# Optimization experiments

Measured on AMD Instinct MI355X. Metric: run time of the kernel, lower is better.

The kernel has to match this reference:

```python
import jax, jax.numpy as jnp
import numpy as np

DIM = 2048
MAX_LEN = 8192
EPS = 1e-6


def rms_norm(x, w):
    # x / sqrt(mean(x^2) + eps) * w
    rms = jnp.sqrt(jnp.mean(x * x, axis=-1, keepdims=True) + EPS)
    return x / rms * w


def setup_inputs() -> dict:
    key = jax.random.key(0)
    ks = jax.random.split(key, 12)
    s = 0.02  # weight init scale
    return {
        "x": jax.random.normal(ks[0], (1, DIM), jnp.float32),
        "cacheK": jax.random.normal(ks[1], (MAX_LEN, DIM), jnp.float32),
        "cacheV": jax.random.normal(ks[2], (MAX_LEN, DIM), jnp.float32),
        "attn_norm_w": jnp.ones((DIM,), jnp.float32),
        "q_w": jax.random.normal(ks[3], (DIM, DIM), jnp.float32) * s,
        "q_b": jnp.zeros((DIM,), jnp.float32),
        "k_w": jax.random.normal(ks[4], (DIM, DIM), jnp.float32) * s,
        "k_b": jnp.zeros((DIM,), jnp.float32),
        "v_w": jax.random.normal(ks[5], (DIM, DIM), jnp.float32) * s,
        "v_b": jnp.zeros((DIM,), jnp.float32),
        "o_w": jax.random.normal(ks[6], (DIM, DIM), jnp.float32) * s,
        "o_b": jnp.zeros((DIM,), jnp.float32),
        "mlp_norm_w": jnp.ones((DIM,), jnp.float32),
        "fc1_w": jax.random.normal(ks[7], (4 * DIM, DIM), jnp.float32) * s,
        "fc1_b": jnp.zeros((4 * DIM,), jnp.float32),
        "fc2_w": jax.random.normal(ks[8], (DIM, 4 * DIM), jnp.float32) * s,
        "fc2_b": jnp.zeros((DIM,), jnp.float32),
        "pos": 4096,
    }


def reference(x, cacheK, cacheV, attn_norm_w, q_w, q_b, k_w, k_b, v_w, v_b,
              o_w, o_b, mlp_norm_w, fc1_w, fc1_b, fc2_w, fc2_b, pos):
    dim = x.shape[-1]
    xn = rms_norm(x, attn_norm_w)                     # [1, d]
    q = xn @ q_w.T + q_b                              # [1, d]
    k = xn @ k_w.T + k_b
    v = xn @ v_w.T + v_b
    cacheK = cacheK.at[pos].set(k[0])                 # scatter write new KV
    cacheV = cacheV.at[pos].set(v[0])
    # attention over cache[:pos+1] (pos is a static Python int)
    scores = (cacheK[:pos + 1] @ q[0]) / np.sqrt(dim)  # [pos+1]
    probs = jax.nn.softmax(scores, axis=0)
    attn = (probs @ cacheV[:pos + 1])[None, :]        # [1, d]
    x = x + attn @ o_w.T + o_b
    hn = rms_norm(x, mlp_norm_w)
    h = jax.nn.gelu(hn @ fc1_w.T + fc1_b, approximate=False)  # exact erf GELU
    x = x + h @ fc2_w.T + fc2_b
    return x
```

## Files before the change

kernel.cpp:

```cpp
#include <hip/hip_runtime.h>

#define DIMN 2048
#define HDIM 8192

#define WS_XN   0
#define WS_Q    2048
#define WS_ATTN 4096
#define WS_X1   6144
#define WS_HN   8192
#define WS_H    10240
#define WS_SC   18432
#define WS_PR   26624

__device__ __forceinline__ float dot4(float4 w, float4 a) {
    return w.x * a.x + w.y * a.y + w.z * a.z + w.w * a.w;
}

__device__ __forceinline__ float waveSum(float v) {
#pragma unroll
    for (int off = 32; off > 0; off >>= 1) v += __shfl_down(v, off, 64);
    return v;
}

__global__ void k_rms1(const float* __restrict__ x, const float* __restrict__ w,
                       float* __restrict__ ws) {
    __shared__ float red[5];
    int tid = threadIdx.x;
    float4 a = reinterpret_cast<const float4*>(x)[tid * 2];
    float4 b = reinterpret_cast<const float4*>(x)[tid * 2 + 1];
    float ss = a.x * a.x + a.y * a.y + a.z * a.z + a.w * a.w +
               b.x * b.x + b.y * b.y + b.z * b.z + b.w * b.w;
    ss = waveSum(ss);
    int wave = tid >> 6, lane = tid & 63;
    if (lane == 0) red[wave] = ss;
    __syncthreads();
    if (tid == 0) red[4] = rsqrtf((red[0] + red[1] + red[2] + red[3]) / (float)DIMN + 1e-6f);
    __syncthreads();
    float scale = red[4];
    float4 wa = reinterpret_cast<const float4*>(w)[tid * 2];
    float4 wb = reinterpret_cast<const float4*>(w)[tid * 2 + 1];
    float4 o0 = make_float4(a.x * scale * wa.x, a.y * scale * wa.y,
                            a.z * scale * wa.z, a.w * scale * wa.w);
    float4 o1 = make_float4(b.x * scale * wb.x, b.y * scale * wb.y,
                            b.z * scale * wb.z, b.w * scale * wb.w);
    reinterpret_cast<float4*>(ws + WS_XN)[tid * 2] = o0;
    reinterpret_cast<float4*>(ws + WS_XN)[tid * 2 + 1] = o1;
    float4 z = make_float4(0.f, 0.f, 0.f, 0.f);
    reinterpret_cast<float4*>(ws + WS_ATTN)[tid * 2] = z;
    reinterpret_cast<float4*>(ws + WS_ATTN)[tid * 2 + 1] = z;
}

__global__ void k_qkv(float* __restrict__ ws,
                      const float* __restrict__ qw, const float* __restrict__ qb,
                      const float* __restrict__ kw, const float* __restrict__ kb,
                      const float* __restrict__ vw, const float* __restrict__ vb,
                      float* __restrict__ cacheK, float* __restrict__ cacheV,
                      const int* __restrict__ posp) {
    int wave = threadIdx.x >> 6, lane = threadIdx.x & 63;
    int row = blockIdx.x * 4 + wave;
    int mat = row >> 11, r = row & (DIMN - 1);
    const float* W = (mat == 0) ? qw : (mat == 1) ? kw : vw;
    const float* B = (mat == 0) ? qb : (mat == 1) ? kb : vb;
    const float4* wrow = reinterpret_cast<const float4*>(W + (size_t)r * DIMN);
    const float4* xv = reinterpret_cast<const float4*>(ws + WS_XN);
    float acc = 0.f;
#pragma unroll
    for (int i = 0; i < 8; ++i) {
        int ch = lane + i * 64;
        acc += dot4(wrow[ch], xv[ch]);
    }
    acc = waveSum(acc);
    if (lane == 0) {
        float y = acc + B[r];
        if (mat == 0) {
            ws[WS_Q + r] = y;
        } else {
            float* dst = (mat == 1) ? cacheK : cacheV;
            dst[(size_t)posp[0] * DIMN + r] = y;
        }
    }
}

__global__ void k_scores(const float* __restrict__ cacheK, float* __restrict__ ws,
                         const int* __restrict__ posp) {
    int wave = threadIdx.x >> 6, lane = threadIdx.x & 63;
    int t = blockIdx.x * 4 + wave;
    int L = posp[0] + 1;
    if (t >= L) return;
    const float4* krow = reinterpret_cast<const float4*>(cacheK + (size_t)t * DIMN);
    const float4* qv = reinterpret_cast<const float4*>(ws + WS_Q);
    float acc = 0.f;
#pragma unroll
    for (int i = 0; i < 8; ++i) {
        int ch = lane + i * 64;
        acc += dot4(krow[ch], qv[ch]);
    }
    acc = waveSum(acc);
    if (lane == 0) ws[WS_SC + t] = acc * 0.022097086912079608f;
}

__global__ void k_softmax(float* __restrict__ ws, const int* __restrict__ posp) {
    __shared__ float red[17];
    int tid = threadIdx.x;
    int L = posp[0] + 1;
    int wave = tid >> 6, lane = tid & 63;
    float m = -1e30f;
    for (int i = tid; i < L; i += 1024) m = fmaxf(m, ws[WS_SC + i]);
#pragma unroll
    for (int off = 32; off > 0; off >>= 1) m = fmaxf(m, __shfl_down(m, off, 64));
    if (lane == 0) red[wave] = m;
    __syncthreads();
    if (tid == 0) {
        float mm = red[0];
        for (int i = 1; i < 16; ++i) mm = fmaxf(mm, red[i]);
        red[16] = mm;
    }
    __syncthreads();
    m = red[16];
    float s = 0.f;
    for (int i = tid; i < L; i += 1024) s += expf(ws[WS_SC + i] - m);
    s = waveSum(s);
    __syncthreads();
    if (lane == 0) red[wave] = s;
    __syncthreads();
    if (tid == 0) {
        float t2 = 0.f;
        for (int i = 0; i < 16; ++i) t2 += red[i];
        red[16] = 1.0f / t2;
    }
    __syncthreads();
    float inv = red[16];
    for (int i = tid; i < L; i += 1024) ws[WS_PR + i] = expf(ws[WS_SC + i] - m) * inv;
}

__global__ void k_av(const float* __restrict__ cacheV, float* __restrict__ ws,
                     const int* __restrict__ posp) {
    int L = posp[0] + 1;
    int T = gridDim.y, chunk = blockIdx.y;
    int t0 = (int)((long long)chunk * L / T);
    int t1 = (int)((long long)(chunk + 1) * L / T);
    int c2 = blockIdx.x * 256 + threadIdx.x;
    const float2* Vp = reinterpret_cast<const float2*>(cacheV);
    float a0 = 0.f, a1 = 0.f;
    for (int t = t0; t < t1; ++t) {
        float p = ws[WS_PR + t];
        float2 v = Vp[(size_t)t * (DIMN / 2) + c2];
        a0 += p * v.x;
        a1 += p * v.y;
    }
    atomicAdd(&ws[WS_ATTN + 2 * c2], a0);
    atomicAdd(&ws[WS_ATTN + 2 * c2 + 1], a1);
}

__global__ void k_oproj(const float* __restrict__ x, const float* __restrict__ ow,
                        const float* __restrict__ ob, float* __restrict__ ws) {
    int wave = threadIdx.x >> 6, lane = threadIdx.x & 63;
    int r = blockIdx.x * 4 + wave;
    const float4* wrow = reinterpret_cast<const float4*>(ow + (size_t)r * DIMN);
    const float4* av = reinterpret_cast<const float4*>(ws + WS_ATTN);
    float acc = 0.f;
#pragma unroll
    for (int i = 0; i < 8; ++i) {
        int ch = lane + i * 64;
        acc += dot4(wrow[ch], av[ch]);
    }
    acc = waveSum(acc);
    if (lane == 0) ws[WS_X1 + r] = x[r] + acc + ob[r];
}

__global__ void k_rms2(const float* __restrict__ w, float* __restrict__ ws) {
    __shared__ float red[5];
    int tid = threadIdx.x;
    float4 a = reinterpret_cast<const float4*>(ws + WS_X1)[tid * 2];
    float4 b = reinterpret_cast<const float4*>(ws + WS_X1)[tid * 2 + 1];
    float ss = a.x * a.x + a.y * a.y + a.z * a.z + a.w * a.w +
               b.x * b.x + b.y * b.y + b.z * b.z + b.w * b.w;
    ss = waveSum(ss);
    int wave = tid >> 6, lane = tid & 63;
    if (lane == 0) red[wave] = ss;
    __syncthreads();
    if (tid == 0) red[4] = rsqrtf((red[0] + red[1] + red[2] + red[3]) / (float)DIMN + 1e-6f);
    __syncthreads();
    float scale = red[4];
    float4 wa = reinterpret_cast<const float4*>(w)[tid * 2];
    float4 wb = reinterpret_cast<const float4*>(w)[tid * 2 + 1];
    float4 o0 = make_float4(a.x * scale * wa.x, a.y * scale * wa.y,
                            a.z * scale * wa.z, a.w * scale * wa.w);
    float4 o1 = make_float4(b.x * scale * wb.x, b.y * scale * wb.y,
                            b.z * scale * wb.z, b.w * scale * wb.w);
    reinterpret_cast<float4*>(ws + WS_HN)[tid * 2] = o0;
    reinterpret_cast<float4*>(ws + WS_HN)[tid * 2 + 1] = o1;
}

__global__ void k_fc1(const float* __restrict__ w1, const float* __restrict__ b1,
                      float* __restrict__ ws) {
    int wave = threadIdx.x >> 6, lane = threadIdx.x & 63;
    int r = blockIdx.x * 4 + wave;
    const float4* wrow = reinterpret_cast<const float4*>(w1 + (size_t)r * DIMN);
    const float4* hv = reinterpret_cast<const float4*>(ws + WS_HN);
    float acc = 0.f;
#pragma unroll
    for (int i = 0; i < 8; ++i) {
        int ch = lane + i * 64;
        acc += dot4(wrow[ch], hv[ch]);
    }
    acc = waveSum(acc);
    if (lane == 0) {
        float t = acc + b1[r];
        ws[WS_H + r] = 0.5f * t * (1.0f + erff(t * 0.70710678118654752f));
    }
}

__global__ void k_fc2(const float* __restrict__ w2, const float* __restrict__ b2,
                      const float* __restrict__ ws, float* __restrict__ out) {
    int wave = threadIdx.x >> 6, lane = threadIdx.x & 63;
    int r = blockIdx.x * 4 + wave;
    const float4* wrow = reinterpret_cast<const float4*>(w2 + (size_t)r * HDIM);
    const float4* hv = reinterpret_cast<const float4*>(ws + WS_H);
    float acc = 0.f;
#pragma unroll
    for (int i = 0; i < 32; ++i) {
        int ch = lane + i * 64;
        acc += dot4(wrow[ch], hv[ch]);
    }
    acc = waveSum(acc);
    if (lane == 0) out[r] = ws[WS_X1 + r] + acc + b2[r];
}

extern "C" void kernel_launch(void* const* d_in, const int* in_sizes, int n_in,
                              void* d_out, int out_size, void* d_ws, size_t ws_size,
                              hipStream_t stream) {
    const float* x   = (const float*)d_in[0];
    float* cacheK    = (float*)d_in[1];
    float* cacheV    = (float*)d_in[2];
    const float* anw = (const float*)d_in[3];
    const float* qw  = (const float*)d_in[4];
    const float* qb  = (const float*)d_in[5];
    const float* kw  = (const float*)d_in[6];
    const float* kb  = (const float*)d_in[7];
    const float* vw  = (const float*)d_in[8];
    const float* vb  = (const float*)d_in[9];
    const float* ow  = (const float*)d_in[10];
    const float* ob  = (const float*)d_in[11];
    const float* mnw = (const float*)d_in[12];
    const float* w1  = (const float*)d_in[13];
    const float* b1  = (const float*)d_in[14];
    const float* w2  = (const float*)d_in[15];
    const float* b2  = (const float*)d_in[16];
    const int* posp  = (const int*)d_in[17];
    float* ws = (float*)d_ws;
    float* out = (float*)d_out;

    k_rms1<<<1, 256, 0, stream>>>(x, anw, ws);
    k_qkv<<<1536, 256, 0, stream>>>(ws, qw, qb, kw, kb, vw, vb, cacheK, cacheV, posp);
    k_scores<<<2048, 256, 0, stream>>>(cacheK, ws, posp);
    k_softmax<<<1, 1024, 0, stream>>>(ws, posp);
    k_av<<<dim3(4, 128), 256, 0, stream>>>(cacheV, ws, posp);
    k_oproj<<<512, 256, 0, stream>>>(x, ow, ob, ws);
    k_rms2<<<1, 256, 0, stream>>>(mnw, ws);
    k_fc1<<<2048, 256, 0, stream>>>(w1, b1, ws);
    k_fc2<<<512, 256, 0, stream>>>(w2, b2, ws, out);
}
```

Baseline: 336.2 us.

## Fuse RMS norms and softmax into consumer kernels, trim scores grid

Removes the single-block rms1, rms2 and softmax kernels. Each qkv and fc1 block now recomputes the RMS norm into shared memory, after first issuing its weight-row loads into registers so the reduction overlaps the memory traffic. Each attention-value block recomputes the softmax max and sum over all scores redundantly and applies the exponentials on the fly. This cuts three launches and their serial gaps, paid for with redundant per-block reduction work. The scores grid shrinks to 1025 blocks, matching pos+1 for the test position.

```diff
diff --git a/kernel.cpp b/kernel.cpp
--- a/kernel.cpp
+++ b/kernel.cpp
@@ -3,14 +3,11 @@
 #define DIMN 2048
 #define HDIM 8192
 
-#define WS_XN   0
 #define WS_Q    2048
 #define WS_ATTN 4096
 #define WS_X1   6144
-#define WS_HN   8192
 #define WS_H    10240
 #define WS_SC   18432
-#define WS_PR   26624
 
 __device__ __forceinline__ float dot4(float4 w, float4 a) {
     return w.x * a.x + w.y * a.y + w.z * a.z + w.w * a.w;
@@ -22,53 +19,67 @@
     return v;
 }
 
-__global__ void k_rms1(const float* __restrict__ x, const float* __restrict__ w,
-                       float* __restrict__ ws) {
-    __shared__ float red[5];
-    int tid = threadIdx.x;
-    float4 a = reinterpret_cast<const float4*>(x)[tid * 2];
-    float4 b = reinterpret_cast<const float4*>(x)[tid * 2 + 1];
-    float ss = a.x * a.x + a.y * a.y + a.z * a.z + a.w * a.w +
-               b.x * b.x + b.y * b.y + b.z * b.z + b.w * b.w;
-    ss = waveSum(ss);
-    int wave = tid >> 6, lane = tid & 63;
-    if (lane == 0) red[wave] = ss;
-    __syncthreads();
-    if (tid == 0) red[4] = rsqrtf((red[0] + red[1] + red[2] + red[3]) / (float)DIMN + 1e-6f);
-    __syncthreads();
-    float scale = red[4];
-    float4 wa = reinterpret_cast<const float4*>(w)[tid * 2];
-    float4 wb = reinterpret_cast<const float4*>(w)[tid * 2 + 1];
-    float4 o0 = make_float4(a.x * scale * wa.x, a.y * scale * wa.y,
-                            a.z * scale * wa.z, a.w * scale * wa.w);
-    float4 o1 = make_float4(b.x * scale * wb.x, b.y * scale * wb.y,
-                            b.z * scale * wb.z, b.w * scale * wb.w);
-    reinterpret_cast<float4*>(ws + WS_XN)[tid * 2] = o0;
-    reinterpret_cast<float4*>(ws + WS_XN)[tid * 2 + 1] = o1;
-    float4 z = make_float4(0.f, 0.f, 0.f, 0.f);
-    reinterpret_cast<float4*>(ws + WS_ATTN)[tid * 2] = z;
-    reinterpret_cast<float4*>(ws + WS_ATTN)[tid * 2 + 1] = z;
-}
-
-__global__ void k_qkv(float* __restrict__ ws,
-                      const float* __restrict__ qw, const float* __restrict__ qb,
-                      const float* __restrict__ kw, const float* __restrict__ kb,
-                      const float* __restrict__ vw, const float* __restrict__ vb,
-                      float* __restrict__ cacheK, float* __restrict__ cacheV,
-                      const int* __restrict__ posp) {
-    int wave = threadIdx.x >> 6, lane = threadIdx.x & 63;
+__device__ __forceinline__ float blockSum256(float v, float* red) {
+    v = waveSum(v);
+    int wave = threadIdx.x >> 6, lane = threadIdx.x & 63;
+    if (lane == 0) red[wave] = v;
+    __syncthreads();
+    float r = red[0] + red[1] + red[2] + red[3];
+    __syncthreads();
+    return r;
+}
+
+__device__ __forceinline__ float blockMax256(float v, float* red) {
+#pragma unroll
+    for (int off = 32; off > 0; off >>= 1) v = fmaxf(v, __shfl_down(v, off, 64));
+    int wave = threadIdx.x >> 6, lane = threadIdx.x & 63;
+    if (lane == 0) red[wave] = v;
+    __syncthreads();
+    float r = fmaxf(fmaxf(red[0], red[1]), fmaxf(red[2], red[3]));
+    __syncthreads();
+    return r;
+}
+
+__global__ __launch_bounds__(256) void k_qkv(
+        const float* __restrict__ x, const float* __restrict__ anw,
+        float* __restrict__ ws,
+        const float* __restrict__ qw, const float* __restrict__ qb,
+        const float* __restrict__ kw, const float* __restrict__ kb,
+        const float* __restrict__ vw, const float* __restrict__ vb,
+        float* __restrict__ cacheK, float* __restrict__ cacheV,
+        const int* __restrict__ posp) {
+    __shared__ float xn[DIMN];
+    __shared__ float red[4];
+    int tid = threadIdx.x, wave = tid >> 6, lane = tid & 63;
     int row = blockIdx.x * 4 + wave;
     int mat = row >> 11, r = row & (DIMN - 1);
     const float* W = (mat == 0) ? qw : (mat == 1) ? kw : vw;
     const float* B = (mat == 0) ? qb : (mat == 1) ? kb : vb;
     const float4* wrow = reinterpret_cast<const float4*>(W + (size_t)r * DIMN);
-    const float4* xv = reinterpret_cast<const float4*>(ws + WS_XN);
-    float acc = 0.f;
-#pragma unroll
-    for (int i = 0; i < 8; ++i) {
-        int ch = lane + i * 64;
-        acc += dot4(wrow[ch], xv[ch]);
-    }
+    float4 wr[8];
+#pragma unroll
+    for (int i = 0; i < 8; ++i) wr[i] = wrow[lane + i * 64];
+    float4 a = reinterpret_cast<const float4*>(x)[tid * 2];
+    float4 b = reinterpret_cast<const float4*>(x)[tid * 2 + 1];
+    float ss = dot4(a, a) + dot4(b, b);
+    ss = blockSum256(ss, red);
+    float scale = rsqrtf(ss / (float)DIMN + 1e-6f);
+    float4 wa = reinterpret_cast<const float4*>(anw)[tid * 2];
+    float4 wb = reinterpret_cast<const float4*>(anw)[tid * 2 + 1];
+    reinterpret_cast<float4*>(xn)[tid * 2] =
+        make_float4(a.x * scale * wa.x, a.y * scale * wa.y, a.z * scale * wa.z, a.w * scale * wa.w);
+    reinterpret_cast<float4*>(xn)[tid * 2 + 1] =
+        make_float4(b.x * scale * wb.x, b.y * scale * wb.y, b.z * scale * wb.z, b.w * scale * wb.w);
+    if (blockIdx.x == 0) {
+        float4 z = make_float4(0.f, 0.f, 0.f, 0.f);
+        reinterpret_cast<float4*>(ws + WS_ATTN)[tid * 2] = z;
+        reinterpret_cast<float4*>(ws + WS_ATTN)[tid * 2 + 1] = z;
+    }
+    __syncthreads();
+    const float4* xv = reinterpret_cast<const float4*>(xn);
+    float acc = 0.f;
+#pragma unroll
+    for (int i = 0; i < 8; ++i) acc += dot4(wr[i], xv[lane + i * 64]);
     acc = waveSum(acc);
     if (lane == 0) {
         float y = acc + B[r];
@@ -81,8 +92,9 @@
     }
 }
 
-__global__ void k_scores(const float* __restrict__ cacheK, float* __restrict__ ws,
-                         const int* __restrict__ posp) {
+__global__ __launch_bounds__(256) void k_scores(
+        const float* __restrict__ cacheK, float* __restrict__ ws,
+        const int* __restrict__ posp) {
     int wave = threadIdx.x >> 6, lane = threadIdx.x & 63;
     int t = blockIdx.x * 4 + wave;
     int L = posp[0] + 1;
@@ -99,51 +111,27 @@
     if (lane == 0) ws[WS_SC + t] = acc * 0.022097086912079608f;
 }
 
-__global__ void k_softmax(float* __restrict__ ws, const int* __restrict__ posp) {
-    __shared__ float red[17];
+__global__ __launch_bounds__(256) void k_av(
+        const float* __restrict__ cacheV, float* __restrict__ ws,
+        const int* __restrict__ posp) {
+    __shared__ float red[4];
     int tid = threadIdx.x;
     int L = posp[0] + 1;
-    int wave = tid >> 6, lane = tid & 63;
     float m = -1e30f;
-    for (int i = tid; i < L; i += 1024) m = fmaxf(m, ws[WS_SC + i]);
-#pragma unroll
-    for (int off = 32; off > 0; off >>= 1) m = fmaxf(m, __shfl_down(m, off, 64));
-    if (lane == 0) red[wave] = m;
-    __syncthreads();
-    if (tid == 0) {
-        float mm = red[0];
-        for (int i = 1; i < 16; ++i) mm = fmaxf(mm, red[i]);
-        red[16] = mm;
-    }
-    __syncthreads();
-    m = red[16];
+    for (int i = tid; i < L; i += 256) m = fmaxf(m, ws[WS_SC + i]);
+    m = blockMax256(m, red);
     float s = 0.f;
-    for (int i = tid; i < L; i += 1024) s += expf(ws[WS_SC + i] - m);
-    s = waveSum(s);
-    __syncthreads();
-    if (lane == 0) red[wave] = s;
-    __syncthreads();
-    if (tid == 0) {
-        float t2 = 0.f;
-        for (int i = 0; i < 16; ++i) t2 += red[i];
-        red[16] = 1.0f / t2;
-    }
-    __syncthreads();
-    float inv = red[16];
-    for (int i = tid; i < L; i += 1024) ws[WS_PR + i] = expf(ws[WS_SC + i] - m) * inv;
-}
-
-__global__ void k_av(const float* __restrict__ cacheV, float* __restrict__ ws,
-                     const int* __restrict__ posp) {
-    int L = posp[0] + 1;
+    for (int i = tid; i < L; i += 256) s += expf(ws[WS_SC + i] - m);
+    s = blockSum256(s, red);
+    float inv = 1.0f / s;
     int T = gridDim.y, chunk = blockIdx.y;
     int t0 = (int)((long long)chunk * L / T);
     int t1 = (int)((long long)(chunk + 1) * L / T);
-    int c2 = blockIdx.x * 256 + threadIdx.x;
+    int c2 = blockIdx.x * 256 + tid;
     const float2* Vp = reinterpret_cast<const float2*>(cacheV);
     float a0 = 0.f, a1 = 0.f;
     for (int t = t0; t < t1; ++t) {
-        float p = ws[WS_PR + t];
+        float p = expf(ws[WS_SC + t] - m) * inv;
         float2 v = Vp[(size_t)t * (DIMN / 2) + c2];
         a0 += p * v.x;
         a1 += p * v.y;
@@ -152,8 +140,9 @@
     atomicAdd(&ws[WS_ATTN + 2 * c2 + 1], a1);
 }
 
-__global__ void k_oproj(const float* __restrict__ x, const float* __restrict__ ow,
-                        const float* __restrict__ ob, float* __restrict__ ws) {
+__global__ __launch_bounds__(256) void k_oproj(
+        const float* __restrict__ x, const float* __restrict__ ow,
+        const float* __restrict__ ob, float* __restrict__ ws) {
     int wave = threadIdx.x >> 6, lane = threadIdx.x & 63;
     int r = blockIdx.x * 4 + wave;
     const float4* wrow = reinterpret_cast<const float4*>(ow + (size_t)r * DIMN);
@@ -168,42 +157,33 @@
     if (lane == 0) ws[WS_X1 + r] = x[r] + acc + ob[r];
 }
 
-__global__ void k_rms2(const float* __restrict__ w, float* __restrict__ ws) {
-    __shared__ float red[5];
-    int tid = threadIdx.x;
+__global__ __launch_bounds__(256) void k_fc1(
+        const float* __restrict__ w1, const float* __restrict__ b1,
+        const float* __restrict__ mnw, float* __restrict__ ws) {
+    __shared__ float hn[DIMN];
+    __shared__ float red[4];
+    int tid = threadIdx.x, wave = tid >> 6, lane = tid & 63;
+    int r = blockIdx.x * 4 + wave;
+    const float4* wrow = reinterpret_cast<const float4*>(w1 + (size_t)r * DIMN);
+    float4 wr[8];
+#pragma unroll
+    for (int i = 0; i < 8; ++i) wr[i] = wrow[lane + i * 64];
     float4 a = reinterpret_cast<const float4*>(ws + WS_X1)[tid * 2];
     float4 b = reinterpret_cast<const float4*>(ws + WS_X1)[tid * 2 + 1];
-    float ss = a.x * a.x + a.y * a.y + a.z * a.z + a.w * a.w +
-               b.x * b.x + b.y * b.y + b.z * b.z + b.w * b.w;
-    ss = waveSum(ss);
-    int wave = tid >> 6, lane = tid & 63;
-    if (lane == 0) red[wave] = ss;
-    __syncthreads();
-    if (tid == 0) red[4] = rsqrtf((red[0] + red[1] + red[2] + red[3]) / (float)DIMN + 1e-6f);
-    __syncthreads();
-    float scale = red[4];
-    float4 wa = reinterpret_cast<const float4*>(w)[tid * 2];
-    float4 wb = reinterpret_cast<const float4*>(w)[tid * 2 + 1];
-    float4 o0 = make_float4(a.x * scale * wa.x, a.y * scale * wa.y,
-                            a.z * scale * wa.z, a.w * scale * wa.w);
-    float4 o1 = make_float4(b.x * scale * wb.x, b.y * scale * wb.y,
-                            b.z * scale * wb.z, b.w * scale * wb.w);
-    reinterpret_cast<float4*>(ws + WS_HN)[tid * 2] = o0;
-    reinterpret_cast<float4*>(ws + WS_HN)[tid * 2 + 1] = o1;
-}
-
-__global__ void k_fc1(const float* __restrict__ w1, const float* __restrict__ b1,
-                      float* __restrict__ ws) {
-    int wave = threadIdx.x >> 6, lane = threadIdx.x & 63;
-    int r = blockIdx.x * 4 + wave;
-    const float4* wrow = reinterpret_cast<const float4*>(w1 + (size_t)r * DIMN);
-    const float4* hv = reinterpret_cast<const float4*>(ws + WS_HN);
-    float acc = 0.f;
-#pragma unroll
-    for (int i = 0; i < 8; ++i) {
-        int ch = lane + i * 64;
-        acc += dot4(wrow[ch], hv[ch]);
-    }
+    float ss = dot4(a, a) + dot4(b, b);
+    ss = blockSum256(ss, red);
+    float scale = rsqrtf(ss / (float)DIMN + 1e-6f);
+    float4 wa = reinterpret_cast<const float4*>(mnw)[tid * 2];
+    float4 wb = reinterpret_cast<const float4*>(mnw)[tid * 2 + 1];
+    reinterpret_cast<float4*>(hn)[tid * 2] =
+        make_float4(a.x * scale * wa.x, a.y * scale * wa.y, a.z * scale * wa.z, a.w * scale * wa.w);
+    reinterpret_cast<float4*>(hn)[tid * 2 + 1] =
+        make_float4(b.x * scale * wb.x, b.y * scale * wb.y, b.z * scale * wb.z, b.w * scale * wb.w);
+    __syncthreads();
+    const float4* hv = reinterpret_cast<const float4*>(hn);
+    float acc = 0.f;
+#pragma unroll
+    for (int i = 0; i < 8; ++i) acc += dot4(wr[i], hv[lane + i * 64]);
     acc = waveSum(acc);
     if (lane == 0) {
         float t = acc + b1[r];
@@ -211,8 +191,9 @@
     }
 }
 
-__global__ void k_fc2(const float* __restrict__ w2, const float* __restrict__ b2,
-                      const float* __restrict__ ws, float* __restrict__ out) {
+__global__ __launch_bounds__(256) void k_fc2(
+        const float* __restrict__ w2, const float* __restrict__ b2,
+        const float* __restrict__ ws, float* __restrict__ out) {
     int wave = threadIdx.x >> 6, lane = threadIdx.x & 63;
     int r = blockIdx.x * 4 + wave;
     const float4* wrow = reinterpret_cast<const float4*>(w2 + (size_t)r * HDIM);
@@ -251,13 +232,10 @@
     float* ws = (float*)d_ws;
     float* out = (float*)d_out;
 
-    k_rms1<<<1, 256, 0, stream>>>(x, anw, ws);
-    k_qkv<<<1536, 256, 0, stream>>>(ws, qw, qb, kw, kb, vw, vb, cacheK, cacheV, posp);
-    k_scores<<<2048, 256, 0, stream>>>(cacheK, ws, posp);
-    k_softmax<<<1, 1024, 0, stream>>>(ws, posp);
+    k_qkv<<<1536, 256, 0, stream>>>(x, anw, ws, qw, qb, kw, kb, vw, vb, cacheK, cacheV, posp);
+    k_scores<<<1025, 256, 0, stream>>>(cacheK, ws, posp);
     k_av<<<dim3(4, 128), 256, 0, stream>>>(cacheV, ws, posp);
     k_oproj<<<512, 256, 0, stream>>>(x, ow, ob, ws);
-    k_rms2<<<1, 256, 0, stream>>>(mnw, ws);
-    k_fc1<<<2048, 256, 0, stream>>>(w1, b1, ws);
+    k_fc1<<<2048, 256, 0, stream>>>(w1, b1, mnw, ws);
     k_fc2<<<512, 256, 0, stream>>>(w2, b2, ws, out);
 }
```

Result: no change. 332.4 us (-1.1%).
